# Optimization experiments

Measured on AMD Instinct MI355X. Metric: run time of the kernel, lower is better.

Reference implementation:

```python
import jax, jax.numpy as jnp
import numpy as np

SCALE = 0.08838834764831845  # 1/sqrt(head_dim=128)


def setup_inputs() -> dict:
    key = jax.random.key(0)
    k0, k1, k2 = jax.random.split(key, 3)
    T, H, HKV, D = 8192, 16, 4, 128        # total_tokens, heads, kv heads, head_dim
    NB, BS = 64, 256                        # num_blocks, block_size (NB*BS == T)
    B, BPS = 4, 8                           # batch, blocks per sequence (seq_len = BPS*BS = 2048)
    return {
        "q": jax.random.normal(k0, (T, H, D), jnp.float32),
        "k": jax.random.normal(k1, (T, HKV, D), jnp.float32),
        "v": jax.random.normal(k2, (T, HKV, D), jnp.float32),
        "k_cache": jnp.zeros((NB, BS, HKV, D), jnp.float32),
        "v_cache": jnp.zeros((NB, BS, HKV, D), jnp.float32),
        "slot_mapping": jnp.arange(T, dtype=jnp.int32),
        "block_tables": jnp.arange(B * BPS, dtype=jnp.int32).reshape(B, BPS),
    }


def reference(q, k, v, k_cache, v_cache, slot_mapping, block_tables):
    T, H, D = q.shape
    HKV = k.shape[1]
    NB, BS = k_cache.shape[0], k_cache.shape[1]
    num_slots = NB * BS

    # --- paged KV-cache store (store_kv_cache_kernel): slot -1 means skip ---
    idx = jnp.where(slot_mapping >= 0, slot_mapping, num_slots)  # out-of-range -> dropped
    kc = k_cache.reshape(num_slots, HKV, D).at[idx].set(k, mode="drop")
    vc = v_cache.reshape(num_slots, HKV, D).at[idx].set(v, mode="drop")

    # --- prefill with block tables: read K/V back through the paged cache ---
    B, BPS = block_tables.shape
    S = BPS * BS  # per-sequence length (equal-length ragged batch)
    k_seq = kc.reshape(NB, BS, HKV, D)[block_tables].reshape(B, S, HKV, D)
    v_seq = vc.reshape(NB, BS, HKV, D)[block_tables].reshape(B, S, HKV, D)

    qb = q.reshape(B, S, H, D)
    G = H // HKV  # GQA group size
    kx = jnp.repeat(k_seq, G, axis=2)  # [B,S,H,D]
    vx = jnp.repeat(v_seq, G, axis=2)

    scores = jnp.einsum("bqhd,bkhd->bhqk", qb, kx) * SCALE
    causal = jnp.tril(jnp.ones((S, S), dtype=bool))
    scores = jnp.where(causal, scores, jnp.finfo(scores.dtype).min)
    p = jax.nn.softmax(scores, axis=-1)
    o = jnp.einsum("bhqk,bkhd->bqhd", p, vx)
    return o.reshape(T, H, D)
```

## Files before the change

kernel.cpp:

```cpp
#include <hip/hip_runtime.h>
#include <hip/hip_bf16.h>

typedef unsigned short u16;
typedef unsigned int u32;
typedef __attribute__((ext_vector_type(8))) short bf16x8;
typedef __attribute__((ext_vector_type(4))) float f32x4;

constexpr int T = 8192, H = 16, HKV = 4, D = 128, NB = 64, BS = 256, B = 4, BPS = 8;
constexpr int S = 2048, G = 4;
constexpr float CEXP = 0.08838834764831845f * 1.4426950408889634f;

constexpr int BQ = 128;
constexpr int BK = 32;
constexpr int PPAD = 40;
constexpr int TOK = 32;
constexpr int QF = 128;
constexpr int QROW = 132;

__device__ __forceinline__ float e2(float x) { return __builtin_amdgcn_exp2f(x); }

__device__ __forceinline__ u32 pk_bf16(float a, float b) {
  __hip_bfloat162 h = __float22bfloat162_rn(float2{a, b});
  u32 r; __builtin_memcpy(&r, &h, 4); return r;
}

__device__ __forceinline__ void dma16(const u16* g, u16* l) {
  __builtin_amdgcn_global_load_lds(
      (const __attribute__((address_space(1))) void*)g,
      (__attribute__((address_space(3))) void*)l, 16, 0, 0);
}

__global__ __launch_bounds__(256) void store_kv(
    const float* __restrict__ k, const float* __restrict__ v,
    u16* __restrict__ kcb, u16* __restrict__ vcb, const int* __restrict__ slot) {
  __shared__ int ls[TOK];
  __shared__ int fastflag;
  __shared__ u16 ldv[TOK * QROW];
  int tid = threadIdx.x;
  int t0 = blockIdx.x * TOK;
  int base = blockIdx.y * QF;
  if (tid < TOK) ls[tid] = slot[t0 + tid];
  if (tid == 0) fastflag = 1;
  __syncthreads();
  int s0 = ls[0];
  if (tid < TOK) {
    bool ok = (ls[tid] == s0 + tid);
    if (tid == 0) ok = ok && (s0 >= 0) && ((s0 & 31) == 0) && (s0 + TOK <= NB * BS);
    if (!ok) fastflag = 0;
  }
#pragma unroll
  for (int i = 0; i < 4; ++i) {
    int f = tid + i * 256;
    int t = f >> 5, c4 = f & 31;
    int st = ls[t];
    float4 k4 = *(const float4*)(k + (size_t)(t0 + t) * (HKV * D) + base + c4 * 4);
    float4 v4 = *(const float4*)(v + (size_t)(t0 + t) * (HKV * D) + base + c4 * 4);
    if (st >= 0 && st < NB * BS) {
      uint2 kb = {pk_bf16(k4.x, k4.y), pk_bf16(k4.z, k4.w)};
      *(uint2*)(kcb + (size_t)st * (HKV * D) + base + c4 * 4) = kb;
    }
    u32* ld = (u32*)&ldv[t * QROW + c4 * 4];
    ld[0] = pk_bf16(v4.x, v4.y);
    ld[1] = pk_bf16(v4.z, v4.w);
  }
  __syncthreads();
  if (fastflag) {
    int blk = s0 >> 8, pos0 = s0 & 255;
#pragma unroll
    for (int i = 0; i < 2; ++i) {
      int f = tid + i * 256;
      int row = f >> 2, c8 = f & 3;
      union { uint4 q; u16 s[8]; } o;
#pragma unroll
      for (int j = 0; j < 8; ++j) o.s[j] = ldv[(c8 * 8 + j) * QROW + row];
      *(uint4*)(vcb + ((size_t)blk * (HKV * D) + base + row) * BS + pos0 + c8 * 8) = o.q;
    }
  } else {
#pragma unroll
    for (int i = 0; i < 16; ++i) {
      int f = tid + i * 256;
      int t = f >> 7, row = f & 127;
      int st = ls[t];
      if (st >= 0 && st < NB * BS)
        vcb[((size_t)(st >> 8) * (HKV * D) + base + row) * BS + (st & 255)] =
            ldv[t * QROW + row];
    }
  }
}

__global__ __launch_bounds__(256, 2) void attn(
    const float* __restrict__ q, const u16* __restrict__ kcb,
    const u16* __restrict__ vcb, const int* __restrict__ bt,
    float* __restrict__ out) {
  __shared__ u16 Kl[2][32 * 128];
  __shared__ u16 Vl[128 * 32];
  __shared__ u16 lp[4][2][16 * PPAD];

  int tid = threadIdx.x;
  int lane = tid & 63;
  int w = __builtin_amdgcn_readfirstlane(tid >> 6);
  int col = lane & 15, quad = lane >> 4;

  int i = (int)blockIdx.x;
  int xcd = i & 7;
  int r_ = i >> 3;
  int j = r_ >> 3;
  int qt = j==0?15: j==1?14: j==2?11: j==3?10: j==4?12: j==5?13: j==6?8: j==7?9:
           j==8?2:  j==9?3:  j==10?6: j==11?7: j==12?1: j==13?0: j==14?5: 4;
  int inner = r_ & 7;
  int p = (xcd << 1) | (inner >> 2);
  int b = p >> 2, hkv = p & 3;
  int h = hkv * G + (inner & 3);

  int qbase = qt * BQ;
  const int* btrow = bt + b * BPS;
  int bt0 = __builtin_amdgcn_readfirstlane(btrow[0]);
  int bt1 = __builtin_amdgcn_readfirstlane(btrow[1]);
  int bt2 = __builtin_amdgcn_readfirstlane(btrow[2]);
  int bt3 = __builtin_amdgcn_readfirstlane(btrow[3]);
  int bt4 = __builtin_amdgcn_readfirstlane(btrow[4]);
  int bt5 = __builtin_amdgcn_readfirstlane(btrow[5]);
  int bt6 = __builtin_amdgcn_readfirstlane(btrow[6]);
  int bt7 = __builtin_amdgcn_readfirstlane(btrow[7]);
  auto selblk = [&](int jj) -> int {
    int s01 = (jj & 1) ? bt1 : bt0, s23 = (jj & 1) ? bt3 : bt2;
    int s45 = (jj & 1) ? bt5 : bt4, s67 = (jj & 1) ? bt7 : bt6;
    int s03 = (jj & 2) ? s23 : s01, s47 = (jj & 2) ? s67 : s45;
    return (jj & 4) ? s47 : s03;
  };

  bf16x8 qf[2][4];
#pragma unroll
  for (int mt = 0; mt < 2; ++mt) {
    int qrow = qbase + w * 32 + mt * 16 + col;
    const float* qp = q + ((size_t)(b * S + qrow) * H + h) * D;
#pragma unroll
    for (int kc = 0; kc < 4; ++kc) {
      float4 a0 = *(const float4*)(qp + kc * 32 + quad * 8);
      float4 a1 = *(const float4*)(qp + kc * 32 + quad * 8 + 4);
      union { bf16x8 v; u32 s[4]; } u;
      u.s[0] = pk_bf16(a0.x, a0.y); u.s[1] = pk_bf16(a0.z, a0.w);
      u.s[2] = pk_bf16(a1.x, a1.y); u.s[3] = pk_bf16(a1.z, a1.w);
      qf[mt][kc] = u.v;
    }
  }

  f32x4 oacc[2][8];
#pragma unroll
  for (int mt = 0; mt < 2; ++mt)
#pragma unroll
    for (int dt = 0; dt < 8; ++dt) oacc[mt][dt] = (f32x4){0.f, 0.f, 0.f, 0.f};
  float lsum[2][4] = {{0.f, 0.f, 0.f, 0.f}, {0.f, 0.f, 0.f, 0.f}};

  int q_hi = qbase + w * 32 + 31;
  int kend = qbase + BQ;

  u32 kOff[2], vOff[2], dmaDst[2];
#pragma unroll
  for (int ii = 0; ii < 2; ++ii) {
    int rK = (w * 2 + ii) * 4 + (lane >> 4), cK = lane & 15;
    kOff[ii] = (u32)(rK * (HKV * D) + ((cK ^ (rK & 7)) * 8));
    int rV = (w * 2 + ii) * 16 + (lane >> 2), cV = lane & 3;
    vOff[ii] = (u32)(rV * BS + ((cV ^ ((rV >> 2) & 3)) * 8));
    dmaDst[ii] = (u32)((w * 2 + ii) * 512);
  }

  const u16* kb = kcb + ((size_t)(bt0 * BS) * HKV + hkv) * D;
  const u16* vb = vcb + ((size_t)bt0 * HKV + hkv) * (size_t)(D * BS);

  int buf = 0;
  dma16(kb + kOff[0], &Kl[0][dmaDst[0]]);
  dma16(kb + kOff[1], &Kl[0][dmaDst[1]]);

  for (int kt = 0; kt < kend; kt += BK) {
    asm volatile("s_waitcnt vmcnt(0)" ::: "memory");
    __builtin_amdgcn_sched_barrier(0);
    __builtin_amdgcn_s_barrier();
    __builtin_amdgcn_sched_barrier(0);

    dma16(vb + vOff[0], &Vl[dmaDst[0]]);
    dma16(vb + vOff[1], &Vl[dmaDst[1]]);

    {
      int ktn = kt + BK;
      const u16 *kbN, *vbN;
      if ((ktn & 255) == 0) {
        int blkN = selblk((ktn >> 8) & 7);
        kbN = kcb + ((size_t)(blkN * BS) * HKV + hkv) * D;
        vbN = vcb + ((size_t)blkN * HKV + hkv) * (size_t)(D * BS);
      } else {
        kbN = kb + BK * HKV * D;
        vbN = vb + BK;
      }
      dma16(kbN + kOff[0], &Kl[buf ^ 1][dmaDst[0]]);
      dma16(kbN + kOff[1], &Kl[buf ^ 1][dmaDst[1]]);
      kb = kbN; vb = vbN;
    }

    bool act = (kt <= q_hi);
    if (act) {
      f32x4 sf[2][2];
      __builtin_amdgcn_s_setprio(1);
#pragma unroll
      for (int n = 0; n < 2; ++n) {
        sf[0][n] = (f32x4){0.f, 0.f, 0.f, 0.f};
        sf[1][n] = (f32x4){0.f, 0.f, 0.f, 0.f};
        int krow = n * 16 + col;
#pragma unroll
        for (int kc = 0; kc < 4; ++kc) {
          bf16x8 kf = *(const bf16x8*)&Kl[buf][krow * 128 + (((kc * 4 + quad) ^ (col & 7)) * 8)];
          sf[0][n] = __builtin_amdgcn_mfma_f32_16x16x32_bf16(qf[0][kc], kf, sf[0][n], 0, 0, 0);
          sf[1][n] = __builtin_amdgcn_mfma_f32_16x16x32_bf16(qf[1][kc], kf, sf[1][n], 0, 0, 0);
        }
      }
      __builtin_amdgcn_s_setprio(0);

#pragma unroll
      for (int mt = 0; mt < 2; ++mt) {
        int q_lo = qbase + w * 32 + mt * 16;
        bool nm = (kt + 31 > q_lo);
#pragma unroll
        for (int r = 0; r < 4; ++r) {
          float p0 = e2(sf[mt][0][r] * CEXP);
          float p1 = e2(sf[mt][1][r] * CEXP);
          if (nm) {
            int qg = q_lo + quad * 4 + r;
            if (kt + col > qg) p0 = 0.f;
            if (kt + 16 + col > qg) p1 = 0.f;
          }
          lsum[mt][r] += p0 + p1;
          u32 pb = pk_bf16(p0, p1);
          u16* dst = &lp[w][mt][(quad * 4 + r) * PPAD + col];
          dst[0] = (u16)(pb & 0xffffu);
          dst[16] = (u16)(pb >> 16);
        }
      }
    }

    asm volatile("s_waitcnt vmcnt(2)" ::: "memory");
    __builtin_amdgcn_sched_barrier(0);
    __builtin_amdgcn_s_barrier();
    __builtin_amdgcn_sched_barrier(0);

    if (act) {
      bf16x8 pf0 = *(const bf16x8*)&lp[w][0][col * PPAD + quad * 8];
      bf16x8 pf1 = *(const bf16x8*)&lp[w][1][col * PPAD + quad * 8];
      __builtin_amdgcn_s_setprio(1);
#pragma unroll
      for (int dt = 0; dt < 8; ++dt) {
        bf16x8 vf = *(const bf16x8*)&Vl[(dt * 16 + col) * 32 + ((quad ^ ((col >> 2) & 3)) * 8)];
        oacc[0][dt] = __builtin_amdgcn_mfma_f32_16x16x32_bf16(pf0, vf, oacc[0][dt], 0, 0, 0);
        oacc[1][dt] = __builtin_amdgcn_mfma_f32_16x16x32_bf16(pf1, vf, oacc[1][dt], 0, 0, 0);
      }
      __builtin_amdgcn_s_setprio(0);
    }
    buf ^= 1;
  }

  asm volatile("s_waitcnt vmcnt(0)" ::: "memory");
  __builtin_amdgcn_sched_barrier(0);

#pragma unroll
  for (int mt = 0; mt < 2; ++mt)
#pragma unroll
    for (int r = 0; r < 4; ++r) {
      float l = lsum[mt][r];
      l += __shfl_xor(l, 1); l += __shfl_xor(l, 2);
      l += __shfl_xor(l, 4); l += __shfl_xor(l, 8);
      float inv = 1.f / l;
      int qg = qbase + w * 32 + mt * 16 + quad * 4 + r;
      size_t ob = ((size_t)(b * S + qg) * H + h) * D;
#pragma unroll
      for (int dt = 0; dt < 8; ++dt)
        out[ob + dt * 16 + col] = oacc[mt][dt][r] * inv;
    }
}

extern "C" void kernel_launch(void* const* d_in, const int* in_sizes, int n_in,
                              void* d_out, int out_size, void* d_ws, size_t ws_size,
                              hipStream_t stream) {
  const float* q = (const float*)d_in[0];
  const float* k = (const float*)d_in[1];
  const float* v = (const float*)d_in[2];
  const int* slot = (const int*)d_in[5];
  const int* bt = (const int*)d_in[6];
  float* out = (float*)d_out;

  size_t need = (size_t)T * HKV * D * sizeof(u16);
  u16* kcb; u16* vcb;
  if (ws_size >= 2 * need) {
    kcb = (u16*)d_ws;
    vcb = (u16*)d_ws + (need / sizeof(u16));
  } else {
    kcb = (u16*)d_in[3];
    vcb = (u16*)d_in[4];
  }

  dim3 sgrid(T / TOK, 4);
  store_kv<<<sgrid, 256, 0, stream>>>(k, v, kcb, vcb, slot);
  attn<<<dim3((S / BQ) * H * B), 256, 0, stream>>>(q, kcb, vcb, bt, out);
}
```

Before: 270.4 us.

## Pair causal query tiles per block with smaller tiles and double-buffered K/V

Query tile size drops from 128 to 64 rows, and each block now processes two complementary causal tiles (31-j and j), so every block does about the same amount of work. The previous hard-coded tile-order table is removed. V is now double-buffered alongside K, with a single barrier per key step instead of two. The P staging buffer is per-wave and is no longer synchronized by a block barrier. Launch bounds ask for 4 blocks per CU. Smaller tiles halve the MFMA work per K/V load, and the higher occupancy target risks register pressure.

```diff
diff --git a/kernel.cpp b/kernel.cpp
--- a/kernel.cpp
+++ b/kernel.cpp
@@ -10,7 +10,7 @@
 constexpr int S = 2048, G = 4;
 constexpr float CEXP = 0.08838834764831845f * 1.4426950408889634f;
 
-constexpr int BQ = 128;
+constexpr int BQ = 64;
 constexpr int BK = 32;
 constexpr int PPAD = 40;
 constexpr int TOK = 32;
@@ -88,13 +88,13 @@
   }
 }
 
-__global__ __launch_bounds__(256, 2) void attn(
+__global__ __launch_bounds__(256, 4) void attn(
     const float* __restrict__ q, const u16* __restrict__ kcb,
     const u16* __restrict__ vcb, const int* __restrict__ bt,
     float* __restrict__ out) {
   __shared__ u16 Kl[2][32 * 128];
-  __shared__ u16 Vl[128 * 32];
-  __shared__ u16 lp[4][2][16 * PPAD];
+  __shared__ u16 Vl[2][128 * 32];
+  __shared__ u16 lp[4][16 * PPAD];
 
   int tid = threadIdx.x;
   int lane = tid & 63;
@@ -105,14 +105,11 @@
   int xcd = i & 7;
   int r_ = i >> 3;
   int j = r_ >> 3;
-  int qt = j==0?15: j==1?14: j==2?11: j==3?10: j==4?12: j==5?13: j==6?8: j==7?9:
-           j==8?2:  j==9?3:  j==10?6: j==11?7: j==12?1: j==13?0: j==14?5: 4;
   int inner = r_ & 7;
   int p = (xcd << 1) | (inner >> 2);
   int b = p >> 2, hkv = p & 3;
   int h = hkv * G + (inner & 3);
 
-  int qbase = qt * BQ;
   const int* btrow = bt + b * BPS;
   int bt0 = __builtin_amdgcn_readfirstlane(btrow[0]);
   int bt1 = __builtin_amdgcn_readfirstlane(btrow[1]);
@@ -129,32 +126,6 @@
     return (jj & 4) ? s47 : s03;
   };
 
-  bf16x8 qf[2][4];
-#pragma unroll
-  for (int mt = 0; mt < 2; ++mt) {
-    int qrow = qbase + w * 32 + mt * 16 + col;
-    const float* qp = q + ((size_t)(b * S + qrow) * H + h) * D;
-#pragma unroll
-    for (int kc = 0; kc < 4; ++kc) {
-      float4 a0 = *(const float4*)(qp + kc * 32 + quad * 8);
-      float4 a1 = *(const float4*)(qp + kc * 32 + quad * 8 + 4);
-      union { bf16x8 v; u32 s[4]; } u;
-      u.s[0] = pk_bf16(a0.x, a0.y); u.s[1] = pk_bf16(a0.z, a0.w);
-      u.s[2] = pk_bf16(a1.x, a1.y); u.s[3] = pk_bf16(a1.z, a1.w);
-      qf[mt][kc] = u.v;
-    }
-  }
-
-  f32x4 oacc[2][8];
-#pragma unroll
-  for (int mt = 0; mt < 2; ++mt)
-#pragma unroll
-    for (int dt = 0; dt < 8; ++dt) oacc[mt][dt] = (f32x4){0.f, 0.f, 0.f, 0.f};
-  float lsum[2][4] = {{0.f, 0.f, 0.f, 0.f}, {0.f, 0.f, 0.f, 0.f}};
-
-  int q_hi = qbase + w * 32 + 31;
-  int kend = qbase + BQ;
-
   u32 kOff[2], vOff[2], dmaDst[2];
 #pragma unroll
   for (int ii = 0; ii < 2; ++ii) {
@@ -165,115 +136,133 @@
     dmaDst[ii] = (u32)((w * 2 + ii) * 512);
   }
 
-  const u16* kb = kcb + ((size_t)(bt0 * BS) * HKV + hkv) * D;
-  const u16* vb = vcb + ((size_t)bt0 * HKV + hkv) * (size_t)(D * BS);
-
-  int buf = 0;
-  dma16(kb + kOff[0], &Kl[0][dmaDst[0]]);
-  dma16(kb + kOff[1], &Kl[0][dmaDst[1]]);
-
-  for (int kt = 0; kt < kend; kt += BK) {
+  auto phase = [&](int qt) {
+    int qbase = qt * BQ;
+
+    bf16x8 qf[4];
+    {
+      int qrow = qbase + w * 16 + col;
+      const float* qp = q + ((size_t)(b * S + qrow) * H + h) * D;
+#pragma unroll
+      for (int kc = 0; kc < 4; ++kc) {
+        float4 a0 = *(const float4*)(qp + kc * 32 + quad * 8);
+        float4 a1 = *(const float4*)(qp + kc * 32 + quad * 8 + 4);
+        union { bf16x8 v; u32 s[4]; } u;
+        u.s[0] = pk_bf16(a0.x, a0.y); u.s[1] = pk_bf16(a0.z, a0.w);
+        u.s[2] = pk_bf16(a1.x, a1.y); u.s[3] = pk_bf16(a1.z, a1.w);
+        qf[kc] = u.v;
+      }
+    }
+
+    f32x4 oacc[8];
+#pragma unroll
+    for (int dt = 0; dt < 8; ++dt) oacc[dt] = (f32x4){0.f, 0.f, 0.f, 0.f};
+    float lsum[4] = {0.f, 0.f, 0.f, 0.f};
+
+    int q_lo = qbase + w * 16;
+    int q_hi = q_lo + 15;
+    int kend = qbase + BQ;
+
+    const u16* kb = kcb + ((size_t)(bt0 * BS) * HKV + hkv) * D;
+    const u16* vb = vcb + ((size_t)bt0 * HKV + hkv) * (size_t)(D * BS);
+
     asm volatile("s_waitcnt vmcnt(0)" ::: "memory");
     __builtin_amdgcn_sched_barrier(0);
     __builtin_amdgcn_s_barrier();
     __builtin_amdgcn_sched_barrier(0);
-
-    dma16(vb + vOff[0], &Vl[dmaDst[0]]);
-    dma16(vb + vOff[1], &Vl[dmaDst[1]]);
-
-    {
-      int ktn = kt + BK;
-      const u16 *kbN, *vbN;
-      if ((ktn & 255) == 0) {
-        int blkN = selblk((ktn >> 8) & 7);
-        kbN = kcb + ((size_t)(blkN * BS) * HKV + hkv) * D;
-        vbN = vcb + ((size_t)blkN * HKV + hkv) * (size_t)(D * BS);
-      } else {
-        kbN = kb + BK * HKV * D;
-        vbN = vb + BK;
+    dma16(kb + kOff[0], &Kl[0][dmaDst[0]]);
+    dma16(kb + kOff[1], &Kl[0][dmaDst[1]]);
+    dma16(vb + vOff[0], &Vl[0][dmaDst[0]]);
+    dma16(vb + vOff[1], &Vl[0][dmaDst[1]]);
+
+    int buf = 0;
+    for (int kt = 0; kt < kend; kt += BK) {
+      asm volatile("s_waitcnt vmcnt(0)" ::: "memory");
+      __builtin_amdgcn_sched_barrier(0);
+      __builtin_amdgcn_s_barrier();
+      __builtin_amdgcn_sched_barrier(0);
+
+      {
+        int ktn = kt + BK;
+        if (ktn < kend) {
+          if ((ktn & 255) == 0) {
+            int blkN = selblk(ktn >> 8);
+            kb = kcb + ((size_t)(blkN * BS) * HKV + hkv) * D;
+            vb = vcb + ((size_t)blkN * HKV + hkv) * (size_t)(D * BS);
+          } else {
+            kb += BK * HKV * D;
+            vb += BK;
+          }
+        }
+        dma16(kb + kOff[0], &Kl[buf ^ 1][dmaDst[0]]);
+        dma16(kb + kOff[1], &Kl[buf ^ 1][dmaDst[1]]);
+        dma16(vb + vOff[0], &Vl[buf ^ 1][dmaDst[0]]);
+        dma16(vb + vOff[1], &Vl[buf ^ 1][dmaDst[1]]);
       }
-      dma16(kbN + kOff[0], &Kl[buf ^ 1][dmaDst[0]]);
-      dma16(kbN + kOff[1], &Kl[buf ^ 1][dmaDst[1]]);
-      kb = kbN; vb = vbN;
-    }
-
-    bool act = (kt <= q_hi);
-    if (act) {
-      f32x4 sf[2][2];
-      __builtin_amdgcn_s_setprio(1);
-#pragma unroll
-      for (int n = 0; n < 2; ++n) {
-        sf[0][n] = (f32x4){0.f, 0.f, 0.f, 0.f};
-        sf[1][n] = (f32x4){0.f, 0.f, 0.f, 0.f};
-        int krow = n * 16 + col;
-#pragma unroll
-        for (int kc = 0; kc < 4; ++kc) {
-          bf16x8 kf = *(const bf16x8*)&Kl[buf][krow * 128 + (((kc * 4 + quad) ^ (col & 7)) * 8)];
-          sf[0][n] = __builtin_amdgcn_mfma_f32_16x16x32_bf16(qf[0][kc], kf, sf[0][n], 0, 0, 0);
-          sf[1][n] = __builtin_amdgcn_mfma_f32_16x16x32_bf16(qf[1][kc], kf, sf[1][n], 0, 0, 0);
-        }
-      }
-      __builtin_amdgcn_s_setprio(0);
-
-#pragma unroll
-      for (int mt = 0; mt < 2; ++mt) {
-        int q_lo = qbase + w * 32 + mt * 16;
+
+      bool act = (kt <= q_hi);
+      if (act) {
+        f32x4 sf[2];
+        __builtin_amdgcn_s_setprio(1);
+#pragma unroll
+        for (int n = 0; n < 2; ++n) {
+          sf[n] = (f32x4){0.f, 0.f, 0.f, 0.f};
+          int krow = n * 16 + col;
+#pragma unroll
+          for (int kc = 0; kc < 4; ++kc) {
+            bf16x8 kf = *(const bf16x8*)&Kl[buf][krow * 128 + (((kc * 4 + quad) ^ (col & 7)) * 8)];
+            sf[n] = __builtin_amdgcn_mfma_f32_16x16x32_bf16(qf[kc], kf, sf[n], 0, 0, 0);
+          }
+        }
+        __builtin_amdgcn_s_setprio(0);
+
         bool nm = (kt + 31 > q_lo);
 #pragma unroll
         for (int r = 0; r < 4; ++r) {
-          float p0 = e2(sf[mt][0][r] * CEXP);
-          float p1 = e2(sf[mt][1][r] * CEXP);
+          float p0 = e2(sf[0][r] * CEXP);
+          float p1 = e2(sf[1][r] * CEXP);
           if (nm) {
             int qg = q_lo + quad * 4 + r;
             if (kt + col > qg) p0 = 0.f;
             if (kt + 16 + col > qg) p1 = 0.f;
           }
-          lsum[mt][r] += p0 + p1;
+          lsum[r] += p0 + p1;
           u32 pb = pk_bf16(p0, p1);
-          u16* dst = &lp[w][mt][(quad * 4 + r) * PPAD + col];
+          u16* dst = &lp[w][(quad * 4 + r) * PPAD + col];
           dst[0] = (u16)(pb & 0xffffu);
           dst[16] = (u16)(pb >> 16);
         }
+
+        bf16x8 pf = *(const bf16x8*)&lp[w][col * PPAD + quad * 8];
+        __builtin_amdgcn_s_setprio(1);
+#pragma unroll
+        for (int dt = 0; dt < 8; ++dt) {
+          bf16x8 vf = *(const bf16x8*)&Vl[buf][(dt * 16 + col) * 32 + ((quad ^ ((col >> 2) & 3)) * 8)];
+          oacc[dt] = __builtin_amdgcn_mfma_f32_16x16x32_bf16(pf, vf, oacc[dt], 0, 0, 0);
+        }
+        __builtin_amdgcn_s_setprio(0);
       }
-    }
-
-    asm volatile("s_waitcnt vmcnt(2)" ::: "memory");
-    __builtin_amdgcn_sched_barrier(0);
-    __builtin_amdgcn_s_barrier();
-    __builtin_amdgcn_sched_barrier(0);
-
-    if (act) {
-      bf16x8 pf0 = *(const bf16x8*)&lp[w][0][col * PPAD + quad * 8];
-      bf16x8 pf1 = *(const bf16x8*)&lp[w][1][col * PPAD + quad * 8];
-      __builtin_amdgcn_s_setprio(1);
-#pragma unroll
-      for (int dt = 0; dt < 8; ++dt) {
-        bf16x8 vf = *(const bf16x8*)&Vl[(dt * 16 + col) * 32 + ((quad ^ ((col >> 2) & 3)) * 8)];
-        oacc[0][dt] = __builtin_amdgcn_mfma_f32_16x16x32_bf16(pf0, vf, oacc[0][dt], 0, 0, 0);
-        oacc[1][dt] = __builtin_amdgcn_mfma_f32_16x16x32_bf16(pf1, vf, oacc[1][dt], 0, 0, 0);
-      }
-      __builtin_amdgcn_s_setprio(0);
-    }
-    buf ^= 1;
-  }
-
-  asm volatile("s_waitcnt vmcnt(0)" ::: "memory");
-  __builtin_amdgcn_sched_barrier(0);
-
-#pragma unroll
-  for (int mt = 0; mt < 2; ++mt)
+      buf ^= 1;
+    }
+
 #pragma unroll
     for (int r = 0; r < 4; ++r) {
-      float l = lsum[mt][r];
+      float l = lsum[r];
       l += __shfl_xor(l, 1); l += __shfl_xor(l, 2);
       l += __shfl_xor(l, 4); l += __shfl_xor(l, 8);
       float inv = 1.f / l;
-      int qg = qbase + w * 32 + mt * 16 + quad * 4 + r;
+      int qg = qbase + w * 16 + quad * 4 + r;
       size_t ob = ((size_t)(b * S + qg) * H + h) * D;
 #pragma unroll
       for (int dt = 0; dt < 8; ++dt)
-        out[ob + dt * 16 + col] = oacc[mt][dt][r] * inv;
-    }
+        out[ob + dt * 16 + col] = oacc[dt][r] * inv;
+    }
+  };
+
+  phase(31 - j);
+  phase(j);
+
+  asm volatile("s_waitcnt vmcnt(0)" ::: "memory");
 }
 
 extern "C" void kernel_launch(void* const* d_in, const int* in_sizes, int n_in,
@@ -298,5 +287,5 @@
 
   dim3 sgrid(T / TOK, 4);
   store_kv<<<sgrid, 256, 0, stream>>>(k, v, kcb, vcb, slot);
-  attn<<<dim3((S / BQ) * H * B), 256, 0, stream>>>(q, kcb, vcb, bt, out);
-}
+  attn<<<dim3((S / (2 * BQ)) * H * B), 256, 0, stream>>>(q, kcb, vcb, bt, out);
+}
```

After: 275.1 us. No clear change (+1.7%).

## Pair causal query tiles per block and double-buffer V with one barrier per step

Applied to the files above, without the earlier changes.

Each block now processes two query tiles, qt=15-j followed by qt=j, so every block does about the same amount of causal work, and the grid is halved. V gets its own double buffer so K and V for the next step are prefetched together. This removes the mid-iteration barrier between softmax and PV, leaving one barrier per K step, and the P padding shrinks to 36. The costs are longer-running blocks, a serialised pipeline restart between the two phases, more LDS use, and possible LDS bank conflicts from the new padding.

```diff
diff --git a/kernel.cpp b/kernel.cpp
--- a/kernel.cpp
+++ b/kernel.cpp
@@ -12,7 +12,7 @@
 
 constexpr int BQ = 128;
 constexpr int BK = 32;
-constexpr int PPAD = 40;
+constexpr int PPAD = 36;
 constexpr int TOK = 32;
 constexpr int QF = 128;
 constexpr int QROW = 132;
@@ -93,7 +93,7 @@
     const u16* __restrict__ vcb, const int* __restrict__ bt,
     float* __restrict__ out) {
   __shared__ u16 Kl[2][32 * 128];
-  __shared__ u16 Vl[128 * 32];
+  __shared__ u16 Vl[2][128 * 32];
   __shared__ u16 lp[4][2][16 * PPAD];
 
   int tid = threadIdx.x;
@@ -105,14 +105,11 @@
   int xcd = i & 7;
   int r_ = i >> 3;
   int j = r_ >> 3;
-  int qt = j==0?15: j==1?14: j==2?11: j==3?10: j==4?12: j==5?13: j==6?8: j==7?9:
-           j==8?2:  j==9?3:  j==10?6: j==11?7: j==12?1: j==13?0: j==14?5: 4;
   int inner = r_ & 7;
   int p = (xcd << 1) | (inner >> 2);
   int b = p >> 2, hkv = p & 3;
   int h = hkv * G + (inner & 3);
 
-  int qbase = qt * BQ;
   const int* btrow = bt + b * BPS;
   int bt0 = __builtin_amdgcn_readfirstlane(btrow[0]);
   int bt1 = __builtin_amdgcn_readfirstlane(btrow[1]);
@@ -129,32 +126,6 @@
     return (jj & 4) ? s47 : s03;
   };
 
-  bf16x8 qf[2][4];
-#pragma unroll
-  for (int mt = 0; mt < 2; ++mt) {
-    int qrow = qbase + w * 32 + mt * 16 + col;
-    const float* qp = q + ((size_t)(b * S + qrow) * H + h) * D;
-#pragma unroll
-    for (int kc = 0; kc < 4; ++kc) {
-      float4 a0 = *(const float4*)(qp + kc * 32 + quad * 8);
-      float4 a1 = *(const float4*)(qp + kc * 32 + quad * 8 + 4);
-      union { bf16x8 v; u32 s[4]; } u;
-      u.s[0] = pk_bf16(a0.x, a0.y); u.s[1] = pk_bf16(a0.z, a0.w);
-      u.s[2] = pk_bf16(a1.x, a1.y); u.s[3] = pk_bf16(a1.z, a1.w);
-      qf[mt][kc] = u.v;
-    }
-  }
-
-  f32x4 oacc[2][8];
-#pragma unroll
-  for (int mt = 0; mt < 2; ++mt)
-#pragma unroll
-    for (int dt = 0; dt < 8; ++dt) oacc[mt][dt] = (f32x4){0.f, 0.f, 0.f, 0.f};
-  float lsum[2][4] = {{0.f, 0.f, 0.f, 0.f}, {0.f, 0.f, 0.f, 0.f}};
-
-  int q_hi = qbase + w * 32 + 31;
-  int kend = qbase + BQ;
-
   u32 kOff[2], vOff[2], dmaDst[2];
 #pragma unroll
   for (int ii = 0; ii < 2; ++ii) {
@@ -165,115 +136,145 @@
     dmaDst[ii] = (u32)((w * 2 + ii) * 512);
   }
 
-  const u16* kb = kcb + ((size_t)(bt0 * BS) * HKV + hkv) * D;
-  const u16* vb = vcb + ((size_t)bt0 * HKV + hkv) * (size_t)(D * BS);
-
-  int buf = 0;
-  dma16(kb + kOff[0], &Kl[0][dmaDst[0]]);
-  dma16(kb + kOff[1], &Kl[0][dmaDst[1]]);
-
-  for (int kt = 0; kt < kend; kt += BK) {
+  auto phase = [&](int qt) {
+    int qbase = qt * BQ;
+
+    bf16x8 qf[2][4];
+#pragma unroll
+    for (int mt = 0; mt < 2; ++mt) {
+      int qrow = qbase + w * 32 + mt * 16 + col;
+      const float* qp = q + ((size_t)(b * S + qrow) * H + h) * D;
+#pragma unroll
+      for (int kc = 0; kc < 4; ++kc) {
+        float4 a0 = *(const float4*)(qp + kc * 32 + quad * 8);
+        float4 a1 = *(const float4*)(qp + kc * 32 + quad * 8 + 4);
+        union { bf16x8 v; u32 s[4]; } u;
+        u.s[0] = pk_bf16(a0.x, a0.y); u.s[1] = pk_bf16(a0.z, a0.w);
+        u.s[2] = pk_bf16(a1.x, a1.y); u.s[3] = pk_bf16(a1.z, a1.w);
+        qf[mt][kc] = u.v;
+      }
+    }
+
+    f32x4 oacc[2][8];
+#pragma unroll
+    for (int mt = 0; mt < 2; ++mt)
+#pragma unroll
+      for (int dt = 0; dt < 8; ++dt) oacc[mt][dt] = (f32x4){0.f, 0.f, 0.f, 0.f};
+    float lsum[2][4] = {{0.f, 0.f, 0.f, 0.f}, {0.f, 0.f, 0.f, 0.f}};
+
+    int q_hi = qbase + w * 32 + 31;
+    int kend = qbase + BQ;
+
+    const u16* kb = kcb + ((size_t)(bt0 * BS) * HKV + hkv) * D;
+    const u16* vb = vcb + ((size_t)bt0 * HKV + hkv) * (size_t)(D * BS);
+
     asm volatile("s_waitcnt vmcnt(0)" ::: "memory");
     __builtin_amdgcn_sched_barrier(0);
     __builtin_amdgcn_s_barrier();
     __builtin_amdgcn_sched_barrier(0);
-
-    dma16(vb + vOff[0], &Vl[dmaDst[0]]);
-    dma16(vb + vOff[1], &Vl[dmaDst[1]]);
-
-    {
-      int ktn = kt + BK;
-      const u16 *kbN, *vbN;
-      if ((ktn & 255) == 0) {
-        int blkN = selblk((ktn >> 8) & 7);
-        kbN = kcb + ((size_t)(blkN * BS) * HKV + hkv) * D;
-        vbN = vcb + ((size_t)blkN * HKV + hkv) * (size_t)(D * BS);
-      } else {
-        kbN = kb + BK * HKV * D;
-        vbN = vb + BK;
+    dma16(kb + kOff[0], &Kl[0][dmaDst[0]]);
+    dma16(kb + kOff[1], &Kl[0][dmaDst[1]]);
+    dma16(vb + vOff[0], &Vl[0][dmaDst[0]]);
+    dma16(vb + vOff[1], &Vl[0][dmaDst[1]]);
+
+    int buf = 0;
+    for (int kt = 0; kt < kend; kt += BK) {
+      asm volatile("s_waitcnt vmcnt(0)" ::: "memory");
+      __builtin_amdgcn_sched_barrier(0);
+      __builtin_amdgcn_s_barrier();
+      __builtin_amdgcn_sched_barrier(0);
+
+      {
+        int ktn = kt + BK;
+        if (ktn < kend) {
+          if ((ktn & 255) == 0) {
+            int blkN = selblk(ktn >> 8);
+            kb = kcb + ((size_t)(blkN * BS) * HKV + hkv) * D;
+            vb = vcb + ((size_t)blkN * HKV + hkv) * (size_t)(D * BS);
+          } else {
+            kb += BK * HKV * D;
+            vb += BK;
+          }
+        }
+        dma16(kb + kOff[0], &Kl[buf ^ 1][dmaDst[0]]);
+        dma16(kb + kOff[1], &Kl[buf ^ 1][dmaDst[1]]);
+        dma16(vb + vOff[0], &Vl[buf ^ 1][dmaDst[0]]);
+        dma16(vb + vOff[1], &Vl[buf ^ 1][dmaDst[1]]);
       }
-      dma16(kbN + kOff[0], &Kl[buf ^ 1][dmaDst[0]]);
-      dma16(kbN + kOff[1], &Kl[buf ^ 1][dmaDst[1]]);
-      kb = kbN; vb = vbN;
-    }
-
-    bool act = (kt <= q_hi);
-    if (act) {
-      f32x4 sf[2][2];
-      __builtin_amdgcn_s_setprio(1);
-#pragma unroll
-      for (int n = 0; n < 2; ++n) {
-        sf[0][n] = (f32x4){0.f, 0.f, 0.f, 0.f};
-        sf[1][n] = (f32x4){0.f, 0.f, 0.f, 0.f};
-        int krow = n * 16 + col;
-#pragma unroll
-        for (int kc = 0; kc < 4; ++kc) {
-          bf16x8 kf = *(const bf16x8*)&Kl[buf][krow * 128 + (((kc * 4 + quad) ^ (col & 7)) * 8)];
-          sf[0][n] = __builtin_amdgcn_mfma_f32_16x16x32_bf16(qf[0][kc], kf, sf[0][n], 0, 0, 0);
-          sf[1][n] = __builtin_amdgcn_mfma_f32_16x16x32_bf16(qf[1][kc], kf, sf[1][n], 0, 0, 0);
+
+      bool act = (kt <= q_hi);
+      if (act) {
+        f32x4 sf[2][2];
+        __builtin_amdgcn_s_setprio(1);
+#pragma unroll
+        for (int n = 0; n < 2; ++n) {
+          sf[0][n] = (f32x4){0.f, 0.f, 0.f, 0.f};
+          sf[1][n] = (f32x4){0.f, 0.f, 0.f, 0.f};
+          int krow = n * 16 + col;
+#pragma unroll
+          for (int kc = 0; kc < 4; ++kc) {
+            bf16x8 kf = *(const bf16x8*)&Kl[buf][krow * 128 + (((kc * 4 + quad) ^ (col & 7)) * 8)];
+            sf[0][n] = __builtin_amdgcn_mfma_f32_16x16x32_bf16(qf[0][kc], kf, sf[0][n], 0, 0, 0);
+            sf[1][n] = __builtin_amdgcn_mfma_f32_16x16x32_bf16(qf[1][kc], kf, sf[1][n], 0, 0, 0);
+          }
         }
+        __builtin_amdgcn_s_setprio(0);
+
+#pragma unroll
+        for (int mt = 0; mt < 2; ++mt) {
+          int q_lo = qbase + w * 32 + mt * 16;
+          bool nm = (kt + 31 > q_lo);
+#pragma unroll
+          for (int r = 0; r < 4; ++r) {
+            float p0 = e2(sf[mt][0][r] * CEXP);
+            float p1 = e2(sf[mt][1][r] * CEXP);
+            if (nm) {
+              int qg = q_lo + quad * 4 + r;
+              if (kt + col > qg) p0 = 0.f;
+              if (kt + 16 + col > qg) p1 = 0.f;
+            }
+            lsum[mt][r] += p0 + p1;
+            u32 pb = pk_bf16(p0, p1);
+            u16* dst = &lp[w][mt][(quad * 4 + r) * PPAD + col];
+            dst[0] = (u16)(pb & 0xffffu);
+            dst[16] = (u16)(pb >> 16);
+          }
+        }
+
+        bf16x8 pf0 = *(const bf16x8*)&lp[w][0][col * PPAD + quad * 8];
+        bf16x8 pf1 = *(const bf16x8*)&lp[w][1][col * PPAD + quad * 8];
+        __builtin_amdgcn_s_setprio(1);
+#pragma unroll
+        for (int dt = 0; dt < 8; ++dt) {
+          bf16x8 vf = *(const bf16x8*)&Vl[buf][(dt * 16 + col) * 32 + ((quad ^ ((col >> 2) & 3)) * 8)];
+          oacc[0][dt] = __builtin_amdgcn_mfma_f32_16x16x32_bf16(pf0, vf, oacc[0][dt], 0, 0, 0);
+          oacc[1][dt] = __builtin_amdgcn_mfma_f32_16x16x32_bf16(pf1, vf, oacc[1][dt], 0, 0, 0);
+        }
+        __builtin_amdgcn_s_setprio(0);
       }
-      __builtin_amdgcn_s_setprio(0);
-
-#pragma unroll
-      for (int mt = 0; mt < 2; ++mt) {
-        int q_lo = qbase + w * 32 + mt * 16;
-        bool nm = (kt + 31 > q_lo);
-#pragma unroll
-        for (int r = 0; r < 4; ++r) {
-          float p0 = e2(sf[mt][0][r] * CEXP);
-          float p1 = e2(sf[mt][1][r] * CEXP);
-          if (nm) {
-            int qg = q_lo + quad * 4 + r;
-            if (kt + col > qg) p0 = 0.f;
-            if (kt + 16 + col > qg) p1 = 0.f;
-          }
-          lsum[mt][r] += p0 + p1;
-          u32 pb = pk_bf16(p0, p1);
-          u16* dst = &lp[w][mt][(quad * 4 + r) * PPAD + col];
-          dst[0] = (u16)(pb & 0xffffu);
-          dst[16] = (u16)(pb >> 16);
-        }
+      buf ^= 1;
+    }
+
+#pragma unroll
+    for (int mt = 0; mt < 2; ++mt)
+#pragma unroll
+      for (int r = 0; r < 4; ++r) {
+        float l = lsum[mt][r];
+        l += __shfl_xor(l, 1); l += __shfl_xor(l, 2);
+        l += __shfl_xor(l, 4); l += __shfl_xor(l, 8);
+        float inv = 1.f / l;
+        int qg = qbase + w * 32 + mt * 16 + quad * 4 + r;
+        size_t ob = ((size_t)(b * S + qg) * H + h) * D;
+#pragma unroll
+        for (int dt = 0; dt < 8; ++dt)
+          out[ob + dt * 16 + col] = oacc[mt][dt][r] * inv;
       }
-    }
-
-    asm volatile("s_waitcnt vmcnt(2)" ::: "memory");
-    __builtin_amdgcn_sched_barrier(0);
-    __builtin_amdgcn_s_barrier();
-    __builtin_amdgcn_sched_barrier(0);
-
-    if (act) {
-      bf16x8 pf0 = *(const bf16x8*)&lp[w][0][col * PPAD + quad * 8];
-      bf16x8 pf1 = *(const bf16x8*)&lp[w][1][col * PPAD + quad * 8];
-      __builtin_amdgcn_s_setprio(1);
-#pragma unroll
-      for (int dt = 0; dt < 8; ++dt) {
-        bf16x8 vf = *(const bf16x8*)&Vl[(dt * 16 + col) * 32 + ((quad ^ ((col >> 2) & 3)) * 8)];
-        oacc[0][dt] = __builtin_amdgcn_mfma_f32_16x16x32_bf16(pf0, vf, oacc[0][dt], 0, 0, 0);
-        oacc[1][dt] = __builtin_amdgcn_mfma_f32_16x16x32_bf16(pf1, vf, oacc[1][dt], 0, 0, 0);
-      }
-      __builtin_amdgcn_s_setprio(0);
-    }
-    buf ^= 1;
-  }
+  };
+
+  phase(15 - j);
+  phase(j);
 
   asm volatile("s_waitcnt vmcnt(0)" ::: "memory");
-  __builtin_amdgcn_sched_barrier(0);
-
-#pragma unroll
-  for (int mt = 0; mt < 2; ++mt)
-#pragma unroll
-    for (int r = 0; r < 4; ++r) {
-      float l = lsum[mt][r];
-      l += __shfl_xor(l, 1); l += __shfl_xor(l, 2);
-      l += __shfl_xor(l, 4); l += __shfl_xor(l, 8);
-      float inv = 1.f / l;
-      int qg = qbase + w * 32 + mt * 16 + quad * 4 + r;
-      size_t ob = ((size_t)(b * S + qg) * H + h) * D;
-#pragma unroll
-      for (int dt = 0; dt < 8; ++dt)
-        out[ob + dt * 16 + col] = oacc[mt][dt][r] * inv;
-    }
 }
 
 extern "C" void kernel_launch(void* const* d_in, const int* in_sizes, int n_in,
@@ -298,5 +299,5 @@
 
   dim3 sgrid(T / TOK, 4);
   store_kv<<<sgrid, 256, 0, stream>>>(k, v, kcb, vcb, slot);
-  attn<<<dim3((S / BQ) * H * B), 256, 0, stream>>>(q, kcb, vcb, bt, out);
-}
+  attn<<<dim3((S / (2 * BQ)) * H * B), 256, 0, stream>>>(q, kcb, vcb, bt, out);
+}
```

Result: no change. 270.6 us (+0.1%).
